# Performance work log

Hardware: AMD Instinct MI355X
Metric: run time of the kernel (lower is better)

Reference implementation:

```python
import jax, jax.numpy as jnp
import numpy as np

B, S, D, M, NQ = 256, 200, 128, 64, 5000
A_TRI, B_TRI, C_TRI = 0.01, 0.05, 0.1  # triangular membership params a,b,c


def setup_inputs():
    key = jax.random.key(0)
    ks = jax.random.split(key, 16)
    g = lambda k, shp: jax.random.normal(k, shp, dtype=jnp.float32) * 0.05
    return dict(
        question_seq=jax.random.randint(ks[0], (B, S), 0, NQ),
        correctness_seq=jax.random.randint(ks[1], (B, S), 0, 2),
        Mk=g(ks[2], (M, D)),
        Mv0=g(ks[3], (M, D)),
        emb_concept=g(ks[4], (NQ, D)),
        emb_interaction=g(ks[5], (2 * NQ, D)),
        Wf=g(ks[6], (D, 2 * D)), bf=jnp.zeros((D,), jnp.float32),
        Wa=g(ks[7], (D, 2 * D)), ba=jnp.zeros((D,), jnp.float32),
        We=g(ks[8], (D, D)), be=jnp.zeros((D,), jnp.float32),
        Wadd=g(ks[9], (D, D)), badd=jnp.zeros((D,), jnp.float32),
        W_ih=g(ks[10], (4 * D, D)), W_hh=g(ks[11], (4 * D, D)),
        b_ih=jnp.zeros((4 * D,), jnp.float32), b_hh=jnp.zeros((4 * D,), jnp.float32),
        hx0=g(ks[12], (1, D)), cx0=g(ks[13], (1, D)),
        Wp=g(ks[14], (1, D)), bp=jnp.zeros((1,), jnp.float32),
    )


def _skvmn(Mk, Mv0, emb_concept, emb_interaction, Wf, bf, Wa, ba, We, be,
           Wadd, badd, W_ih, W_hh, b_ih, b_hh, hx0, cx0, Wp, bp,
           question_seq, correctness_seq):
    concept = emb_concept[question_seq]                                # [B,S,D]
    inter = emb_interaction[question_seq + NQ * correctness_seq]        # [B,S,D]

    # ---- DKVMN key addressing + value memory read/erase/add recurrence ----
    def mem_step(mem, xs):
        k_t, y_t = xs                                                   # [B,D]
        cw = jax.nn.softmax(k_t @ Mk.T, axis=1)                         # [B,M]
        read = jnp.einsum('bm,bmd->bd', cw, mem)                        # [B,D]
        f = jnp.tanh(jnp.concatenate([read, k_t], 1) @ Wf.T + bf)       # [B,D]
        we = jnp.concatenate([f, y_t], 1) @ Wa.T + ba                   # write embed
        erase = jax.nn.sigmoid(we @ We.T + be)
        add = jnp.tanh(we @ Wadd.T + badd)
        mem = mem * (1.0 - cw[:, :, None] * erase[:, None, :]) \
              + cw[:, :, None] * add[:, None, :]
        return mem, (cw, f)

    mem0 = jnp.broadcast_to(Mv0[None], (B, M, D)).astype(jnp.float32)
    _, (w, ft) = jax.lax.scan(
        mem_step, mem0,
        (concept.transpose(1, 0, 2), inter.transpose(1, 0, 2)))
    # w: [S,B,M], ft: [S,B,D]

    # ---- triangular layer: bin correlation weights into identity vectors ----
    wb = w.transpose(1, 0, 2)                                           # [B,S,M]
    tri = jnp.minimum((wb - A_TRI) / (B_TRI - A_TRI),
                      (C_TRI - wb) / (C_TRI - B_TRI))
    tri = jnp.maximum(tri, 0.0)
    iv = jnp.where(tri >= 0.6, 2.0, jnp.where(tri >= 0.1, 1.0, 0.0))    # [B,S,M]

    sq = jnp.sum(iv * iv, axis=2)                                       # [B,S]
    dist = sq[:, :, None] + sq[:, None, :] - 2.0 * jnp.einsum('btm,bjm->btj', iv, iv)
    NEG = jnp.float32(-1e32)
    d2 = jnp.where(dist > 0.0, NEG, dist)
    triu = jnp.triu(jnp.ones((S, S), bool), k=0)                        # mask j >= t
    d2 = jnp.where(triu[None], NEG, d2)
    idx_mat = jnp.arange(S * S, dtype=jnp.float32).reshape(S, S)
    score = d2 + idx_mat[None]                                          # [B,S,S]
    prev_t = jnp.argmax(score, axis=2)                                  # [B,S] prior matching step
    valid = jnp.max(score, axis=2) >= 0.0                               # [B,S]

    # ---- hop-LSTM: substitute hx with hidden state of prior matching step ----
    def lstm_step(carry, xs):
        hx, cx, H = carry
        t, x_t, prev_b, valid_b = xs
        h_prev = H[prev_b, jnp.arange(B)]                               # gather [B,D]
        hx = jnp.where(valid_b[:, None], h_prev, hx)
        gates = x_t @ W_ih.T + b_ih + hx @ W_hh.T + b_hh
        i_, f_, g_, o_ = jnp.split(gates, 4, axis=1)
        cx = jax.nn.sigmoid(f_) * cx + jax.nn.sigmoid(i_) * jnp.tanh(g_)
        hx = jax.nn.sigmoid(o_) * jnp.tanh(cx)
        H = jax.lax.dynamic_update_slice(H, hx[None], (t, 0, 0))
        return (hx, cx, H), hx

    H0 = jnp.zeros((S, B, D), jnp.float32)
    hx = jnp.broadcast_to(hx0, (B, D)).astype(jnp.float32)
    cx = jnp.broadcast_to(cx0, (B, D)).astype(jnp.float32)
    _, hs = jax.lax.scan(lstm_step, (hx, cx, H0),
                         (jnp.arange(S), ft, prev_t.T, valid.T))         # hs: [S,B,D]

    logits = jnp.einsum('sbd,d->sb', hs, Wp[0]) + bp[0]
    return jax.nn.sigmoid(logits).T                                     # [B,S]


def reference(question_seq, correctness_seq, Mk, Mv0, emb_concept, emb_interaction,
              Wf, bf, Wa, ba, We, be, Wadd, badd, W_ih, W_hh, b_ih, b_hh,
              hx0, cx0, Wp, bp):
    return _skvmn(Mk, Mv0, emb_concept, emb_interaction, Wf, bf, Wa, ba, We, be,
                  Wadd, badd, W_ih, W_hh, b_ih, b_hh, hx0, cx0, Wp, bp,
                  question_seq, correctness_seq)
```

## Files before the change

### kernel.cpp

```cpp
#include <hip/hip_runtime.h>

typedef unsigned int u32;
typedef unsigned short u16;
typedef unsigned long long u64;
typedef _Float16 f16;
typedef _Float16 f16x2 __attribute__((ext_vector_type(2)));

#define Bn 256
#define Sn 200
#define Dn 128
#define Mn 64
#define NQn 5000

__device__ __forceinline__ float fdot2f(u32 w, u32 x, float acc) {
#if __has_builtin(__builtin_amdgcn_fdot2)
    return __builtin_amdgcn_fdot2(__builtin_bit_cast(f16x2, w),
                                  __builtin_bit_cast(f16x2, x), acc, false);
#else
    f16x2 a = __builtin_bit_cast(f16x2, w);
    f16x2 b = __builtin_bit_cast(f16x2, x);
    return acc + (float)a[0] * (float)b[0] + (float)a[1] * (float)b[1];
#endif
}

__device__ __forceinline__ u32 packh2(float a, float b) {
    u16 ua = __builtin_bit_cast(u16, (f16)a);
    u16 ub = __builtin_bit_cast(u16, (f16)b);
    return (u32)ua | ((u32)ub << 16);
}

__device__ __forceinline__ float h2f(u16 u) { return (float)__builtin_bit_cast(f16, u); }

__device__ __forceinline__ float fexp2f(float x) {
#if __has_builtin(__builtin_amdgcn_exp2f)
    return __builtin_amdgcn_exp2f(x);
#else
    return exp2f(x);
#endif
}
__device__ __forceinline__ float frcpf(float x) {
#if __has_builtin(__builtin_amdgcn_rcpf)
    return __builtin_amdgcn_rcpf(x);
#else
    return 1.0f / x;
#endif
}
__device__ __forceinline__ float sig_fast(float x)  { return frcpf(1.0f + fexp2f(-1.44269504f * x)); }
__device__ __forceinline__ float tanh_fast(float x) { return fmaf(-2.0f, frcpf(1.0f + fexp2f(2.88539008f * x)), 1.0f); }

__device__ __forceinline__ float sigf(float x) { return 1.0f / (1.0f + expf(-x)); }

__global__ __launch_bounds__(512) void phase0_kernel(
    const int* __restrict__ qseq,
    const float* __restrict__ Mk, const float* __restrict__ embc,
    u16* __restrict__ cw16, ulonglong2* __restrict__ codes)
{
    __shared__ float MkT[Dn * 65];
    __shared__ float kb[8][Dn];
    int tid = threadIdx.x;
    for (int idx = tid; idx < Mn * Dn; idx += 512) {
        int m = idx >> 7, d = idx & 127;
        MkT[d * 65 + m] = Mk[idx];
    }
    __syncthreads();
    int w = tid >> 6, lane = tid & 63;
    int item = blockIdx.x * 8 + w;
    int qq = qseq[item];
    kb[w][lane]      = embc[qq * Dn + lane];
    kb[w][lane + 64] = embc[qq * Dn + lane + 64];
    __syncthreads();
    float acc = 0.0f;
    const float* kw = kb[w];
#pragma unroll 8
    for (int d = 0; d < Dn; ++d)
        acc = fmaf(MkT[d * 65 + lane], kw[d], acc);
    float mx = acc;
    for (int off = 32; off; off >>= 1) mx = fmaxf(mx, __shfl_xor(mx, off));
    float e = expf(acc - mx);
    float sm = e;
    for (int off = 32; off; off >>= 1) sm += __shfl_xor(sm, off);
    float cw = e / sm;
    cw16[item * Mn + lane] = __builtin_bit_cast(u16, (f16)cw);
    float t1 = (cw - 0.01f) / (0.05f - 0.01f);
    float t2 = (0.1f - cw) / (0.1f - 0.05f);
    float tri = fminf(t1, t2);
    tri = fmaxf(tri, 0.0f);
    int iv = (tri >= 0.6f) ? 2 : ((tri >= 0.1f) ? 1 : 0);
    u64 b1 = __ballot(iv >= 1);
    u64 b2 = __ballot(iv == 2);
    if (lane == 0) { codes[item].x = b1; codes[item].y = b2; }
}

__global__ __launch_bounds__(256) void match_kernel(
    const ulonglong2* __restrict__ codes, int* __restrict__ prev)
{
    __shared__ u64 clo[Sn], chi[Sn];
    int b = blockIdx.x, tid = threadIdx.x;
    if (tid < Sn) { ulonglong2 c = codes[b * Sn + tid]; clo[tid] = c.x; chi[tid] = c.y; }
    __syncthreads();
    if (tid < Sn) {
        u64 mylo = clo[tid], myhi = chi[tid];
        int best = -1;
        for (int j = 0; j < tid; ++j)
            if (clo[j] == mylo && chi[j] == myhi) best = j;
        prev[b * Sn + tid] = best;
    }
}

__global__ __launch_bounds__(512) void pre_kernel(
    const float* __restrict__ W, const float* __restrict__ emb,
    const int* __restrict__ qseq, const int* __restrict__ cseq, int mode,
    u16* __restrict__ outp)
{
    __shared__ u32 wL[128 * 65];
    __shared__ u32 vb[8][64];
    int tid = threadIdx.x;
    for (int idx = tid; idx < 128 * 64; idx += 512) {
        int dd = idx >> 6, jj = idx & 63;
        const float2 wv = *(const float2*)(W + dd * 256 + 128 + 2 * jj);
        wL[dd * 65 + jj] = packh2(wv.x, wv.y);
    }
    int w = tid >> 6, lane = tid & 63;
    int item = blockIdx.x * 8 + w;
    int row = qseq[item];
    if (mode) row += NQn * cseq[item];
    {
        const float2 kv = *(const float2*)(emb + row * Dn + 2 * lane);
        vb[w][lane] = packh2(kv.x, kv.y);
    }
    __syncthreads();
    const u32* w0 = wL + lane * 65;
    const u32* w1 = wL + (64 + lane) * 65;
    const u32* x  = vb[w];
    float a0 = 0, a1 = 0, b0 = 0, b1 = 0;
#pragma unroll
    for (int jj = 0; jj < 64; jj += 2) {
        a0 = fdot2f(w0[jj],     x[jj],     a0);
        a1 = fdot2f(w0[jj + 1], x[jj + 1], a1);
        b0 = fdot2f(w1[jj],     x[jj],     b0);
        b1 = fdot2f(w1[jj + 1], x[jj + 1], b1);
    }
    outp[item * Dn + lane]      = __builtin_bit_cast(u16, (f16)(a0 + a1));
    outp[item * Dn + 64 + lane] = __builtin_bit_cast(u16, (f16)(b0 + b1));
}

__global__ __launch_bounds__(512, 2) void memrec_kernel(
    const float* __restrict__ Mv0,
    const float* __restrict__ Wf, const float* __restrict__ bfv,
    const float* __restrict__ Wa, const float* __restrict__ bav,
    const float* __restrict__ We, const float* __restrict__ bev,
    const float* __restrict__ Wadd, const float* __restrict__ badv,
    const u16* __restrict__ cw16, const u16* __restrict__ kf16,
    const u16* __restrict__ ya16, u16* __restrict__ ft16)
{
    __shared__ u32 cwL[Sn * 32];
    __shared__ __align__(16) u32 kfb[2][16 * 64];
    __shared__ __align__(16) u32 yab[2][16 * 64];
    __shared__ __align__(16) u32 rbuf[64], fbuf[64], wbuf[64];
    __shared__ float bfL[Dn], baL[Dn], beL[Dn], badL[Dn];

    int tid = threadIdx.x;
    int d = tid >> 2, q = tid & 3;
    int b = blockIdx.x;

    u32 wfr[16], waf[16], wew[16], wadw[16];
    {
        const float2* wf2r = (const float2*)(Wf + d * 256 + q * 32);
        const float2* wa2f = (const float2*)(Wa + d * 256 + q * 32);
        const float2* we2  = (const float2*)(We + d * 128 + q * 32);
        const float2* wd2  = (const float2*)(Wadd + d * 128 + q * 32);
#pragma unroll
        for (int i = 0; i < 16; ++i) {
            float2 a;
            a = wf2r[i]; wfr[i]  = packh2(a.x, a.y);
            a = wa2f[i]; waf[i]  = packh2(a.x, a.y);
            a = we2[i];  wew[i]  = packh2(a.x, a.y);
            a = wd2[i];  wadw[i] = packh2(a.x, a.y);
        }
    }
    float memv[16];
#pragma unroll
    for (int i = 0; i < 16; ++i) memv[i] = Mv0[(q * 16 + i) * Dn + d];

    if (tid < Dn) { bfL[tid] = bfv[tid]; baL[tid] = bav[tid]; beL[tid] = bev[tid]; badL[tid] = badv[tid]; }

    for (int i = tid; i < Sn * 32; i += 512) cwL[i] = ((const u32*)cw16)[b * Sn * 32 + i];
    {
        const u32* kg = (const u32*)kf16 + (size_t)(b * Sn) * 64;
        const u32* yg = (const u32*)ya16 + (size_t)(b * Sn) * 64;
        for (int i = tid; i < 1024; i += 512) { kfb[0][i] = kg[i]; yab[0][i] = yg[i]; }
    }
    __syncthreads();

    float cwreg[16];
#pragma unroll
    for (int i = 0; i < 8; ++i) {
        u32 v = cwL[q * 8 + i];
        cwreg[2 * i]     = h2f((u16)(v & 0xffff));
        cwreg[2 * i + 1] = h2f((u16)(v >> 16));
    }

    for (int t = 0; t < Sn; ++t) {
        int sl = (t >> 4) & 1, ti = t & 15;
        if (ti == 0) {
            int c1 = (t >> 4) + 1;
            if (c1 * 16 < Sn) {
                int n = (Sn - c1 * 16 < 16 ? Sn - c1 * 16 : 16) * 64;
                const u32* kg = (const u32*)kf16 + (size_t)(b * Sn + c1 * 16) * 64;
                const u32* yg = (const u32*)ya16 + (size_t)(b * Sn + c1 * 16) * 64;
                for (int i = tid; i < n; i += 512) { kfb[sl ^ 1][i] = kg[i]; yab[sl ^ 1][i] = yg[i]; }
            }
        }
        float p0 = 0, p1 = 0, p2 = 0, p3 = 0;
#pragma unroll
        for (int i = 0; i < 4; ++i) {
            p0 = fmaf(cwreg[i],      memv[i],      p0);
            p1 = fmaf(cwreg[4 + i],  memv[4 + i],  p1);
            p2 = fmaf(cwreg[8 + i],  memv[8 + i],  p2);
            p3 = fmaf(cwreg[12 + i], memv[12 + i], p3);
        }
        float pr = (p0 + p1) + (p2 + p3);
        pr += __shfl_xor(pr, 1);
        pr += __shfl_xor(pr, 2);
        if (q == 0) ((f16*)rbuf)[d] = (f16)pr;
        __syncthreads();
        u16 kfc = ((const u16*)(kfb[sl]))[ti * 128 + d];
        float a0 = 0, a1 = 0, a2 = 0, a3 = 0;
#pragma unroll
        for (int u = 0; u < 4; ++u) {
            uint4 x = ((const uint4*)rbuf)[(q << 2) + u];
            a0 = fdot2f(wfr[4 * u + 0], x.x, a0);
            a1 = fdot2f(wfr[4 * u + 1], x.y, a1);
            a2 = fdot2f(wfr[4 * u + 2], x.z, a2);
            a3 = fdot2f(wfr[4 * u + 3], x.w, a3);
        }
        float accf = (a0 + a1) + (a2 + a3);
        accf += __shfl_xor(accf, 1);
        accf += __shfl_xor(accf, 2);
        float fv = tanh_fast(accf + h2f(kfc) + bfL[d]);
        if (q == 0) ((f16*)fbuf)[d] = (f16)fv;
        if (q == 1) ft16[(size_t)(b * Sn + t) * Dn + d] = __builtin_bit_cast(u16, (f16)fv);
        __syncthreads();
        u16 yac = ((const u16*)(yab[sl]))[ti * 128 + d];
        float c0 = 0, c1_ = 0, c2 = 0, c3 = 0;
#pragma unroll
        for (int u = 0; u < 4; ++u) {
            uint4 x = ((const uint4*)fbuf)[(q << 2) + u];
            c0  = fdot2f(waf[4 * u + 0], x.x, c0);
            c1_ = fdot2f(waf[4 * u + 1], x.y, c1_);
            c2  = fdot2f(waf[4 * u + 2], x.z, c2);
            c3  = fdot2f(waf[4 * u + 3], x.w, c3);
        }
        float accw = (c0 + c1_) + (c2 + c3);
        accw += __shfl_xor(accw, 1);
        accw += __shfl_xor(accw, 2);
        if (q == 0) ((f16*)wbuf)[d] = (f16)(accw + h2f(yac) + baL[d]);
        __syncthreads();
        float e0 = 0, e1 = 0, g0 = 0, g1 = 0;
#pragma unroll
        for (int u = 0; u < 4; ++u) {
            uint4 x = ((const uint4*)wbuf)[(q << 2) + u];
            e0 = fdot2f(wew[4 * u + 0], x.x, e0);   g0 = fdot2f(wadw[4 * u + 0], x.x, g0);
            e1 = fdot2f(wew[4 * u + 1], x.y, e1);   g1 = fdot2f(wadw[4 * u + 1], x.y, g1);
            e0 = fdot2f(wew[4 * u + 2], x.z, e0);   g0 = fdot2f(wadw[4 * u + 2], x.z, g0);
            e1 = fdot2f(wew[4 * u + 3], x.w, e1);   g1 = fdot2f(wadw[4 * u + 3], x.w, g1);
        }
        float pe = e0 + e1, pa = g0 + g1;
        pe += __shfl_xor(pe, 1); pe += __shfl_xor(pe, 2);
        pa += __shfl_xor(pa, 1); pa += __shfl_xor(pa, 2);
        float ev = sig_fast(pe + beL[d]);
        float av = tanh_fast(pa + badL[d]);
        u32 cwn[8];
        if (t + 1 < Sn) {
#pragma unroll
            for (int i = 0; i < 8; ++i) cwn[i] = cwL[(t + 1) * 32 + q * 8 + i];
        }
#pragma unroll
        for (int i = 0; i < 16; ++i) {
            float tt = fmaf(-ev, memv[i], av);
            memv[i] = fmaf(cwreg[i], tt, memv[i]);
        }
        if (t + 1 < Sn) {
#pragma unroll
            for (int i = 0; i < 8; ++i) {
                cwreg[2 * i]     = h2f((u16)(cwn[i] & 0xffff));
                cwreg[2 * i + 1] = h2f((u16)(cwn[i] >> 16));
            }
        }
    }
}

__global__ __launch_bounds__(512, 2) void lstm_kernel(
    const float* __restrict__ W_ih, const float* __restrict__ W_hh,
    const float* __restrict__ b_ih, const float* __restrict__ b_hh,
    const float* __restrict__ hx0, const float* __restrict__ cx0,
    const float* __restrict__ Wp, const float* __restrict__ bp,
    const u16* __restrict__ ft16, const int* __restrict__ prev,
    float* __restrict__ out)
{
    __shared__ u32 HL[(Sn + 1) * 64];
    __shared__ __align__(16) u32 ftb[2][16 * 64];
    __shared__ float gbuf[512];
    __shared__ float bsum[512];
    __shared__ int prevL[Sn];
    __shared__ u32 wpL[64];
    __shared__ float bpL;

    int tid = threadIdx.x, b = blockIdx.x;
    u32 wih[64], whh[64];
    {
        const float2* wi2 = (const float2*)(W_ih + tid * Dn);
        const float2* wh2 = (const float2*)(W_hh + tid * Dn);
#pragma unroll
        for (int i = 0; i < 64; ++i) {
            float2 a;
            a = wi2[i]; wih[i] = packh2(a.x, a.y);
            a = wh2[i]; whh[i] = packh2(a.x, a.y);
        }
    }
    bsum[tid] = b_ih[tid] + b_hh[tid];
    if (tid < 64) {
        HL[tid]  = packh2(hx0[2 * tid], hx0[2 * tid + 1]);
        wpL[tid] = packh2(Wp[2 * tid], Wp[2 * tid + 1]);
    }
    if (tid < Sn) prevL[tid] = prev[b * Sn + tid];
    if (tid == 0) bpL = bp[0];
    float cx = (tid < Dn) ? cx0[tid] : 0.0f;
    {
        const u32* fg = (const u32*)ft16 + (size_t)(b * Sn) * 64;
        for (int i = tid; i < 1024; i += 512) ftb[0][i] = fg[i];
    }
    __syncthreads();

    for (int t = 0; t < Sn; ++t) {
        int sl = (t >> 4) & 1, ti = t & 15;
        if (ti == 0) {
            int c1 = (t >> 4) + 1;
            if (c1 * 16 < Sn) {
                int n = (Sn - c1 * 16 < 16 ? Sn - c1 * 16 : 16) * 64;
                const u32* fg = (const u32*)ft16 + (size_t)(b * Sn + c1 * 16) * 64;
                for (int i = tid; i < n; i += 512) ftb[sl ^ 1][i] = fg[i];
            }
        }
        int pv = prevL[t];
        int hrow = (pv >= 0) ? (pv + 1) : t;
        const uint4* h4 = (const uint4*)(HL + hrow * 64);
        const uint4* f4 = (const uint4*)(ftb[sl] + ti * 64);
        float a0 = bsum[tid], a1 = 0, a2 = 0, a3 = 0;
        float b0 = 0, b1 = 0, b2 = 0, b3 = 0;
#pragma unroll
        for (int u = 0; u < 4; ++u) {
            uint4 x = f4[u];
            a0 = fdot2f(wih[4 * u + 0], x.x, a0);
            a1 = fdot2f(wih[4 * u + 1], x.y, a1);
            a2 = fdot2f(wih[4 * u + 2], x.z, a2);
            a3 = fdot2f(wih[4 * u + 3], x.w, a3);
            uint4 y = h4[u];
            b0 = fdot2f(whh[4 * u + 0], y.x, b0);
            b1 = fdot2f(whh[4 * u + 1], y.y, b1);
            b2 = fdot2f(whh[4 * u + 2], y.z, b2);
            b3 = fdot2f(whh[4 * u + 3], y.w, b3);
        }
        gbuf[tid] = ((a0 + a1) + (a2 + a3)) + ((b0 + b1) + (b2 + b3));
        __syncthreads();
        if (tid < 128) {
            float ig = sig_fast(gbuf[tid]);
            float fg = sig_fast(gbuf[128 + tid]);
            float gg = tanh_fast(gbuf[256 + tid]);
            float og = sig_fast(gbuf[384 + tid]);
            cx = fmaf(fg, cx, ig * gg);
            float h = og * tanh_fast(cx);
            ((f16*)HL)[(t + 1) * Dn + tid] = (f16)h;
        }
        __syncthreads();
    }
    if (tid < Sn) {
        float acc = 0.0f;
        const u32* hr = HL + (tid + 1) * 64;
#pragma unroll 16
        for (int j = 0; j < 64; ++j) acc = fdot2f(hr[j], wpL[j], acc);
        out[b * Sn + tid] = sig_fast(acc + bpL);
    }
}

extern "C" void kernel_launch(void* const* d_in, const int* in_sizes, int n_in,
                              void* d_out, int out_size, void* d_ws, size_t ws_size,
                              hipStream_t stream) {
    const int*   qseq = (const int*)d_in[0];
    const int*   cseq = (const int*)d_in[1];
    const float* Mk   = (const float*)d_in[2];
    const float* Mv0  = (const float*)d_in[3];
    const float* embc = (const float*)d_in[4];
    const float* embi = (const float*)d_in[5];
    const float* Wf   = (const float*)d_in[6];
    const float* bfv  = (const float*)d_in[7];
    const float* Wa   = (const float*)d_in[8];
    const float* bav  = (const float*)d_in[9];
    const float* We   = (const float*)d_in[10];
    const float* bev  = (const float*)d_in[11];
    const float* Wadd = (const float*)d_in[12];
    const float* badv = (const float*)d_in[13];
    const float* W_ih = (const float*)d_in[14];
    const float* W_hh = (const float*)d_in[15];
    const float* b_ih = (const float*)d_in[16];
    const float* b_hh = (const float*)d_in[17];
    const float* hx0  = (const float*)d_in[18];
    const float* cx0  = (const float*)d_in[19];
    const float* Wp   = (const float*)d_in[20];
    const float* bp   = (const float*)d_in[21];
    float* out = (float*)d_out;

    char* ws = (char*)d_ws;
    u16* cw16 = (u16*)ws;
    u16* ft16 = (u16*)(ws + 6553600);
    ulonglong2* codes = (ulonglong2*)(ws + 19660800);
    int* prev = (int*)(ws + 20480000);
    u16* kf16 = (u16*)(ws + 20684800);
    u16* ya16 = (u16*)(ws + 33792000);

    phase0_kernel<<<(Bn * Sn) / 8, 512, 0, stream>>>(qseq, Mk, embc, cw16, codes);
    pre_kernel<<<(Bn * Sn) / 8, 512, 0, stream>>>(Wf, embc, qseq, cseq, 0, kf16);
    pre_kernel<<<(Bn * Sn) / 8, 512, 0, stream>>>(Wa, embi, qseq, cseq, 1, ya16);
    match_kernel<<<Bn, 256, 0, stream>>>(codes, prev);
    memrec_kernel<<<Bn, 512, 0, stream>>>(Mv0, Wf, bfv, Wa, bav, We, bev, Wadd, badv,
                                          cw16, kf16, ya16, ft16);
    lstm_kernel<<<Bn, 512, 0, stream>>>(W_ih, W_hh, b_ih, b_hh, hx0, cx0, Wp, bp,
                                        ft16, prev, out);
}
```

Measured before the change: 628.9 us.

## Fold Wa into erase/add weights, precompute per-vocab rows, restructure LSTM gates

Precomputes We·Wa and Wadd·Wa products so the memory recurrence skips the write-embed matvec and one barrier per step. The input-dependent projections are computed once per vocabulary row rather than per (batch, step) item, then gathered by index inside the recurrence. The LSTM kernel now splits each hidden unit across four lanes holding all four gates, reducing with shuffles so the gate staging buffer and one barrier per step go away. Risks include extra fp16 rounding from the folded matrices and gathers that no longer coalesce.

Measured after the change: 638.9 us. Within noise of the previous version (+1.6%).

```diff
diff --git a/kernel.cpp b/kernel.cpp
--- a/kernel.cpp
+++ b/kernel.cpp
@@ -47,8 +47,6 @@
 }
 __device__ __forceinline__ float sig_fast(float x)  { return frcpf(1.0f + fexp2f(-1.44269504f * x)); }
 __device__ __forceinline__ float tanh_fast(float x) { return fmaf(-2.0f, frcpf(1.0f + fexp2f(2.88539008f * x)), 1.0f); }
-
-__device__ __forceinline__ float sigf(float x) { return 1.0f / (1.0f + expf(-x)); }
 
 __global__ __launch_bounds__(512) void phase0_kernel(
     const int* __restrict__ qseq,
@@ -107,9 +105,40 @@
     }
 }
 
-__global__ __launch_bounds__(512) void pre_kernel(
+__global__ __launch_bounds__(512) void setup_kernel(
+    const float* __restrict__ Wa, const float* __restrict__ We,
+    const float* __restrict__ Wadd,
+    const float* __restrict__ ba, const float* __restrict__ be,
+    const float* __restrict__ badd,
+    float* __restrict__ CEf, float* __restrict__ CAf,
+    float* __restrict__ CEy, float* __restrict__ CAy,
+    float* __restrict__ c0s)
+{
+    __shared__ float weR[128], waR[128];
+    int d = blockIdx.x, tid = threadIdx.x;
+    if (tid < 128) weR[tid] = We[d * 128 + tid];
+    else if (tid < 256) waR[tid - 128] = Wadd[d * 128 + (tid - 128)];
+    __syncthreads();
+    int mat = tid >> 7, j = tid & 127;
+    const float* src = (mat == 0 || mat == 2) ? weR : waR;
+    int col = (mat < 2) ? j : (128 + j);
+    float acc = 0.0f;
+    for (int k = 0; k < 128; ++k) acc = fmaf(src[k], Wa[k * 256 + col], acc);
+    float* dst = (mat == 0) ? CEf : (mat == 1) ? CAf : (mat == 2) ? CEy : CAy;
+    dst[d * 128 + j] = acc;
+    if (tid == 0) {
+        float a = 0.0f;
+        for (int k = 0; k < 128; ++k) a = fmaf(weR[k], ba[k], a);
+        c0s[d] = a + be[d];
+    } else if (tid == 1) {
+        float a = 0.0f;
+        for (int k = 0; k < 128; ++k) a = fmaf(waR[k], ba[k], a);
+        c0s[128 + d] = a + badd[d];
+    }
+}
+
+__global__ __launch_bounds__(512) void rowk_kernel(
     const float* __restrict__ W, const float* __restrict__ emb,
-    const int* __restrict__ qseq, const int* __restrict__ cseq, int mode,
     u16* __restrict__ outp)
 {
     __shared__ u32 wL[128 * 65];
@@ -121,9 +150,7 @@
         wL[dd * 65 + jj] = packh2(wv.x, wv.y);
     }
     int w = tid >> 6, lane = tid & 63;
-    int item = blockIdx.x * 8 + w;
-    int row = qseq[item];
-    if (mode) row += NQn * cseq[item];
+    int row = blockIdx.x * 8 + w;
     {
         const float2 kv = *(const float2*)(emb + row * Dn + 2 * lane);
         vb[w][lane] = packh2(kv.x, kv.y);
@@ -140,55 +167,111 @@
         b0 = fdot2f(w1[jj],     x[jj],     b0);
         b1 = fdot2f(w1[jj + 1], x[jj + 1], b1);
     }
-    outp[item * Dn + lane]      = __builtin_bit_cast(u16, (f16)(a0 + a1));
-    outp[item * Dn + 64 + lane] = __builtin_bit_cast(u16, (f16)(b0 + b1));
+    outp[row * Dn + lane]      = __builtin_bit_cast(u16, (f16)(a0 + a1));
+    outp[row * Dn + 64 + lane] = __builtin_bit_cast(u16, (f16)(b0 + b1));
+}
+
+__global__ __launch_bounds__(512) void rowe_kernel(
+    const float* __restrict__ CEy, const float* __restrict__ CAy,
+    const float* __restrict__ c0s, const float* __restrict__ embi,
+    u16* __restrict__ ebR, u16* __restrict__ abR)
+{
+    __shared__ u32 eL[128 * 65];
+    __shared__ u32 aL[128 * 65];
+    __shared__ u32 vb[8][64];
+    __shared__ float c0L[256];
+    int tid = threadIdx.x;
+    for (int idx = tid; idx < 128 * 64; idx += 512) {
+        int dd = idx >> 6, jj = idx & 63;
+        const float2 e2 = *(const float2*)(CEy + dd * 128 + 2 * jj);
+        const float2 a2 = *(const float2*)(CAy + dd * 128 + 2 * jj);
+        eL[dd * 65 + jj] = packh2(e2.x, e2.y);
+        aL[dd * 65 + jj] = packh2(a2.x, a2.y);
+    }
+    if (tid < 256) c0L[tid] = c0s[tid];
+    int w = tid >> 6, lane = tid & 63;
+    int row = blockIdx.x * 8 + w;
+    {
+        const float2 kv = *(const float2*)(embi + row * Dn + 2 * lane);
+        vb[w][lane] = packh2(kv.x, kv.y);
+    }
+    __syncthreads();
+    const u32* x   = vb[w];
+    const u32* e0p = eL + lane * 65;
+    const u32* e1p = eL + (64 + lane) * 65;
+    const u32* a0p = aL + lane * 65;
+    const u32* a1p = aL + (64 + lane) * 65;
+    float ea0 = 0, ea1 = 0, eb0 = 0, eb1 = 0;
+    float aa0 = 0, aa1 = 0, ab0 = 0, ab1 = 0;
+#pragma unroll
+    for (int jj = 0; jj < 64; jj += 2) {
+        ea0 = fdot2f(e0p[jj],     x[jj],     ea0);
+        ea1 = fdot2f(e0p[jj + 1], x[jj + 1], ea1);
+        eb0 = fdot2f(e1p[jj],     x[jj],     eb0);
+        eb1 = fdot2f(e1p[jj + 1], x[jj + 1], eb1);
+        aa0 = fdot2f(a0p[jj],     x[jj],     aa0);
+        aa1 = fdot2f(a0p[jj + 1], x[jj + 1], aa1);
+        ab0 = fdot2f(a1p[jj],     x[jj],     ab0);
+        ab1 = fdot2f(a1p[jj + 1], x[jj + 1], ab1);
+    }
+    ebR[row * Dn + lane]      = __builtin_bit_cast(u16, (f16)(ea0 + ea1 + c0L[lane]));
+    ebR[row * Dn + 64 + lane] = __builtin_bit_cast(u16, (f16)(eb0 + eb1 + c0L[64 + lane]));
+    abR[row * Dn + lane]      = __builtin_bit_cast(u16, (f16)(aa0 + aa1 + c0L[128 + lane]));
+    abR[row * Dn + 64 + lane] = __builtin_bit_cast(u16, (f16)(ab0 + ab1 + c0L[192 + lane]));
 }
 
 __global__ __launch_bounds__(512, 2) void memrec_kernel(
     const float* __restrict__ Mv0,
     const float* __restrict__ Wf, const float* __restrict__ bfv,
-    const float* __restrict__ Wa, const float* __restrict__ bav,
-    const float* __restrict__ We, const float* __restrict__ bev,
-    const float* __restrict__ Wadd, const float* __restrict__ badv,
-    const u16* __restrict__ cw16, const u16* __restrict__ kf16,
-    const u16* __restrict__ ya16, u16* __restrict__ ft16)
+    const float* __restrict__ CEf, const float* __restrict__ CAf,
+    const u16* __restrict__ cw16, const u16* __restrict__ kfR,
+    const u16* __restrict__ ebR, const u16* __restrict__ abR,
+    const int* __restrict__ qseq, const int* __restrict__ cseq,
+    u16* __restrict__ ft16)
 {
     __shared__ u32 cwL[Sn * 32];
     __shared__ __align__(16) u32 kfb[2][16 * 64];
-    __shared__ __align__(16) u32 yab[2][16 * 64];
-    __shared__ __align__(16) u32 rbuf[64], fbuf[64], wbuf[64];
-    __shared__ float bfL[Dn], baL[Dn], beL[Dn], badL[Dn];
+    __shared__ __align__(16) u32 ebb[2][16 * 64];
+    __shared__ __align__(16) u32 abb[2][16 * 64];
+    __shared__ __align__(16) u32 rbuf[64], fbuf[64];
+    __shared__ float bfL[Dn];
+    __shared__ int qrowL[Sn], irowL[Sn];
 
     int tid = threadIdx.x;
     int d = tid >> 2, q = tid & 3;
     int b = blockIdx.x;
 
-    u32 wfr[16], waf[16], wew[16], wadw[16];
+    u32 wfr[16], wew[16], wadw[16];
     {
-        const float2* wf2r = (const float2*)(Wf + d * 256 + q * 32);
-        const float2* wa2f = (const float2*)(Wa + d * 256 + q * 32);
-        const float2* we2  = (const float2*)(We + d * 128 + q * 32);
-        const float2* wd2  = (const float2*)(Wadd + d * 128 + q * 32);
+        const float2* wf2 = (const float2*)(Wf  + d * 256 + q * 32);
+        const float2* we2 = (const float2*)(CEf + d * 128 + q * 32);
+        const float2* wd2 = (const float2*)(CAf + d * 128 + q * 32);
 #pragma unroll
         for (int i = 0; i < 16; ++i) {
             float2 a;
-            a = wf2r[i]; wfr[i]  = packh2(a.x, a.y);
-            a = wa2f[i]; waf[i]  = packh2(a.x, a.y);
-            a = we2[i];  wew[i]  = packh2(a.x, a.y);
-            a = wd2[i];  wadw[i] = packh2(a.x, a.y);
+            a = wf2[i]; wfr[i]  = packh2(a.x, a.y);
+            a = we2[i]; wew[i]  = packh2(a.x, a.y);
+            a = wd2[i]; wadw[i] = packh2(a.x, a.y);
         }
     }
     float memv[16];
 #pragma unroll
     for (int i = 0; i < 16; ++i) memv[i] = Mv0[(q * 16 + i) * Dn + d];
 
-    if (tid < Dn) { bfL[tid] = bfv[tid]; baL[tid] = bav[tid]; beL[tid] = bev[tid]; badL[tid] = badv[tid]; }
+    if (tid < Dn) bfL[tid] = bfv[tid];
+    if (tid < Sn) {
+        int qq = qseq[b * Sn + tid];
+        qrowL[tid] = qq;
+        irowL[tid] = qq + NQn * cseq[b * Sn + tid];
+    }
+    __syncthreads();
 
     for (int i = tid; i < Sn * 32; i += 512) cwL[i] = ((const u32*)cw16)[b * Sn * 32 + i];
-    {
-        const u32* kg = (const u32*)kf16 + (size_t)(b * Sn) * 64;
-        const u32* yg = (const u32*)ya16 + (size_t)(b * Sn) * 64;
-        for (int i = tid; i < 1024; i += 512) { kfb[0][i] = kg[i]; yab[0][i] = yg[i]; }
+    for (int i = tid; i < 1024; i += 512) {
+        int s = i >> 6, off = i & 63;
+        kfb[0][i] = ((const u32*)kfR)[qrowL[s] * 64 + off];
+        ebb[0][i] = ((const u32*)ebR)[irowL[s] * 64 + off];
+        abb[0][i] = ((const u32*)abR)[irowL[s] * 64 + off];
     }
     __syncthreads();
 
@@ -206,9 +289,13 @@
             int c1 = (t >> 4) + 1;
             if (c1 * 16 < Sn) {
                 int n = (Sn - c1 * 16 < 16 ? Sn - c1 * 16 : 16) * 64;
-                const u32* kg = (const u32*)kf16 + (size_t)(b * Sn + c1 * 16) * 64;
-                const u32* yg = (const u32*)ya16 + (size_t)(b * Sn + c1 * 16) * 64;
-                for (int i = tid; i < n; i += 512) { kfb[sl ^ 1][i] = kg[i]; yab[sl ^ 1][i] = yg[i]; }
+                for (int i = tid; i < n; i += 512) {
+                    int s = i >> 6, off = i & 63;
+                    int t2 = c1 * 16 + s;
+                    kfb[sl ^ 1][i] = ((const u32*)kfR)[qrowL[t2] * 64 + off];
+                    ebb[sl ^ 1][i] = ((const u32*)ebR)[irowL[t2] * 64 + off];
+                    abb[sl ^ 1][i] = ((const u32*)abR)[irowL[t2] * 64 + off];
+                }
             }
         }
         float p0 = 0, p1 = 0, p2 = 0, p3 = 0;
@@ -225,6 +312,8 @@
         if (q == 0) ((f16*)rbuf)[d] = (f16)pr;
         __syncthreads();
         u16 kfc = ((const u16*)(kfb[sl]))[ti * 128 + d];
+        u16 ebc = ((const u16*)(ebb[sl]))[ti * 128 + d];
+        u16 abc = ((const u16*)(abb[sl]))[ti * 128 + d];
         float a0 = 0, a1 = 0, a2 = 0, a3 = 0;
 #pragma unroll
         for (int u = 0; u < 4; ++u) {
@@ -241,25 +330,10 @@
         if (q == 0) ((f16*)fbuf)[d] = (f16)fv;
         if (q == 1) ft16[(size_t)(b * Sn + t) * Dn + d] = __builtin_bit_cast(u16, (f16)fv);
         __syncthreads();
-        u16 yac = ((const u16*)(yab[sl]))[ti * 128 + d];
-        float c0 = 0, c1_ = 0, c2 = 0, c3 = 0;
+        float e0 = 0, e1 = 0, g0 = 0, g1 = 0;
 #pragma unroll
         for (int u = 0; u < 4; ++u) {
             uint4 x = ((const uint4*)fbuf)[(q << 2) + u];
-            c0  = fdot2f(waf[4 * u + 0], x.x, c0);
-            c1_ = fdot2f(waf[4 * u + 1], x.y, c1_);
-            c2  = fdot2f(waf[4 * u + 2], x.z, c2);
-            c3  = fdot2f(waf[4 * u + 3], x.w, c3);
-        }
-        float accw = (c0 + c1_) + (c2 + c3);
-        accw += __shfl_xor(accw, 1);
-        accw += __shfl_xor(accw, 2);
-        if (q == 0) ((f16*)wbuf)[d] = (f16)(accw + h2f(yac) + baL[d]);
-        __syncthreads();
-        float e0 = 0, e1 = 0, g0 = 0, g1 = 0;
-#pragma unroll
-        for (int u = 0; u < 4; ++u) {
-            uint4 x = ((const uint4*)wbuf)[(q << 2) + u];
             e0 = fdot2f(wew[4 * u + 0], x.x, e0);   g0 = fdot2f(wadw[4 * u + 0], x.x, g0);
             e1 = fdot2f(wew[4 * u + 1], x.y, e1);   g1 = fdot2f(wadw[4 * u + 1], x.y, g1);
             e0 = fdot2f(wew[4 * u + 2], x.z, e0);   g0 = fdot2f(wadw[4 * u + 2], x.z, g0);
@@ -268,8 +342,8 @@
         float pe = e0 + e1, pa = g0 + g1;
         pe += __shfl_xor(pe, 1); pe += __shfl_xor(pe, 2);
         pa += __shfl_xor(pa, 1); pa += __shfl_xor(pa, 2);
-        float ev = sig_fast(pe + beL[d]);
-        float av = tanh_fast(pa + badL[d]);
+        float ev = sig_fast(pe + h2f(ebc));
+        float av = tanh_fast(pa + h2f(abc));
         u32 cwn[8];
         if (t + 1 < Sn) {
 #pragma unroll
@@ -298,34 +372,35 @@
     const u16* __restrict__ ft16, const int* __restrict__ prev,
     float* __restrict__ out)
 {
-    __shared__ u32 HL[(Sn + 1) * 64];
+    __shared__ __align__(16) u32 HL[(Sn + 1) * 64];
     __shared__ __align__(16) u32 ftb[2][16 * 64];
-    __shared__ float gbuf[512];
-    __shared__ float bsum[512];
     __shared__ int prevL[Sn];
     __shared__ u32 wpL[64];
     __shared__ float bpL;
 
     int tid = threadIdx.x, b = blockIdx.x;
-    u32 wih[64], whh[64];
-    {
-        const float2* wi2 = (const float2*)(W_ih + tid * Dn);
-        const float2* wh2 = (const float2*)(W_hh + tid * Dn);
-#pragma unroll
-        for (int i = 0; i < 64; ++i) {
+    int d = tid >> 2, q = tid & 3;
+    u32 wx[4][16], wh[4][16];
+    float bias[4];
+#pragma unroll
+    for (int g = 0; g < 4; ++g) {
+        const float2* wi2 = (const float2*)(W_ih + (size_t)(g * 128 + d) * Dn + q * 32);
+        const float2* wh2 = (const float2*)(W_hh + (size_t)(g * 128 + d) * Dn + q * 32);
+#pragma unroll
+        for (int i = 0; i < 16; ++i) {
             float2 a;
-            a = wi2[i]; wih[i] = packh2(a.x, a.y);
-            a = wh2[i]; whh[i] = packh2(a.x, a.y);
-        }
-    }
-    bsum[tid] = b_ih[tid] + b_hh[tid];
+            a = wi2[i]; wx[g][i] = packh2(a.x, a.y);
+            a = wh2[i]; wh[g][i] = packh2(a.x, a.y);
+        }
+        bias[g] = b_ih[g * 128 + d] + b_hh[g * 128 + d];
+    }
     if (tid < 64) {
         HL[tid]  = packh2(hx0[2 * tid], hx0[2 * tid + 1]);
         wpL[tid] = packh2(Wp[2 * tid], Wp[2 * tid + 1]);
     }
     if (tid < Sn) prevL[tid] = prev[b * Sn + tid];
     if (tid == 0) bpL = bp[0];
-    float cx = (tid < Dn) ? cx0[tid] : 0.0f;
+    float cx = cx0[d];
     {
         const u32* fg = (const u32*)ft16 + (size_t)(b * Sn) * 64;
         for (int i = tid; i < 1024; i += 512) ftb[0][i] = fg[i];
@@ -344,34 +419,38 @@
         }
         int pv = prevL[t];
         int hrow = (pv >= 0) ? (pv + 1) : t;
-        const uint4* h4 = (const uint4*)(HL + hrow * 64);
-        const uint4* f4 = (const uint4*)(ftb[sl] + ti * 64);
-        float a0 = bsum[tid], a1 = 0, a2 = 0, a3 = 0;
-        float b0 = 0, b1 = 0, b2 = 0, b3 = 0;
-#pragma unroll
-        for (int u = 0; u < 4; ++u) {
-            uint4 x = f4[u];
-            a0 = fdot2f(wih[4 * u + 0], x.x, a0);
-            a1 = fdot2f(wih[4 * u + 1], x.y, a1);
-            a2 = fdot2f(wih[4 * u + 2], x.z, a2);
-            a3 = fdot2f(wih[4 * u + 3], x.w, a3);
-            uint4 y = h4[u];
-            b0 = fdot2f(whh[4 * u + 0], y.x, b0);
-            b1 = fdot2f(whh[4 * u + 1], y.y, b1);
-            b2 = fdot2f(whh[4 * u + 2], y.z, b2);
-            b3 = fdot2f(whh[4 * u + 3], y.w, b3);
-        }
-        gbuf[tid] = ((a0 + a1) + (a2 + a3)) + ((b0 + b1) + (b2 + b3));
-        __syncthreads();
-        if (tid < 128) {
-            float ig = sig_fast(gbuf[tid]);
-            float fg = sig_fast(gbuf[128 + tid]);
-            float gg = tanh_fast(gbuf[256 + tid]);
-            float og = sig_fast(gbuf[384 + tid]);
-            cx = fmaf(fg, cx, ig * gg);
-            float h = og * tanh_fast(cx);
-            ((f16*)HL)[(t + 1) * Dn + tid] = (f16)h;
-        }
+        const uint4* h4 = (const uint4*)(HL + hrow * 64 + q * 16);
+        const uint4* f4 = (const uint4*)(ftb[sl] + ti * 64 + q * 16);
+        uint4 xv[4], yv[4];
+#pragma unroll
+        for (int u = 0; u < 4; ++u) { xv[u] = f4[u]; yv[u] = h4[u]; }
+        float gacc[4];
+#pragma unroll
+        for (int g = 0; g < 4; ++g) {
+            float s0 = 0, s1 = 0, s2 = 0, s3 = 0;
+#pragma unroll
+            for (int u = 0; u < 4; ++u) {
+                s0 = fdot2f(wx[g][4 * u + 0], xv[u].x, s0);
+                s1 = fdot2f(wx[g][4 * u + 1], xv[u].y, s1);
+                s2 = fdot2f(wx[g][4 * u + 2], xv[u].z, s2);
+                s3 = fdot2f(wx[g][4 * u + 3], xv[u].w, s3);
+                s0 = fdot2f(wh[g][4 * u + 0], yv[u].x, s0);
+                s1 = fdot2f(wh[g][4 * u + 1], yv[u].y, s1);
+                s2 = fdot2f(wh[g][4 * u + 2], yv[u].z, s2);
+                s3 = fdot2f(wh[g][4 * u + 3], yv[u].w, s3);
+            }
+            float s = (s0 + s1) + (s2 + s3);
+            s += __shfl_xor(s, 1);
+            s += __shfl_xor(s, 2);
+            gacc[g] = s + bias[g];
+        }
+        float ig = sig_fast(gacc[0]);
+        float fgt = sig_fast(gacc[1]);
+        float gg = tanh_fast(gacc[2]);
+        float og = sig_fast(gacc[3]);
+        cx = fmaf(fgt, cx, ig * gg);
+        float h = og * tanh_fast(cx);
+        if (q == 0) ((f16*)HL)[(t + 1) * Dn + d] = (f16)h;
         __syncthreads();
     }
     if (tid < Sn) {
@@ -415,15 +494,23 @@
     u16* ft16 = (u16*)(ws + 6553600);
     ulonglong2* codes = (ulonglong2*)(ws + 19660800);
     int* prev = (int*)(ws + 20480000);
-    u16* kf16 = (u16*)(ws + 20684800);
-    u16* ya16 = (u16*)(ws + 33792000);
-
+    u16* kfR  = (u16*)(ws + 20684800);
+    u16* ebR  = (u16*)(ws + 21964800);
+    u16* abR  = (u16*)(ws + 24524800);
+    float* CEf = (float*)(ws + 27084800);
+    float* CAf = (float*)(ws + 27150336);
+    float* CEy = (float*)(ws + 27215872);
+    float* CAy = (float*)(ws + 27281408);
+    float* c0s = (float*)(ws + 27346944);
+
+    setup_kernel<<<128, 512, 0, stream>>>(Wa, We, Wadd, bav, bev, badv,
+                                          CEf, CAf, CEy, CAy, c0s);
     phase0_kernel<<<(Bn * Sn) / 8, 512, 0, stream>>>(qseq, Mk, embc, cw16, codes);
-    pre_kernel<<<(Bn * Sn) / 8, 512, 0, stream>>>(Wf, embc, qseq, cseq, 0, kf16);
-    pre_kernel<<<(Bn * Sn) / 8, 512, 0, stream>>>(Wa, embi, qseq, cseq, 1, ya16);
+    rowk_kernel<<<NQn / 8, 512, 0, stream>>>(Wf, embc, kfR);
+    rowe_kernel<<<(2 * NQn) / 8, 512, 0, stream>>>(CEy, CAy, c0s, embi, ebR, abR);
     match_kernel<<<Bn, 256, 0, stream>>>(codes, prev);
-    memrec_kernel<<<Bn, 512, 0, stream>>>(Mv0, Wf, bfv, Wa, bav, We, bev, Wadd, badv,
-                                          cw16, kf16, ya16, ft16);
+    memrec_kernel<<<Bn, 512, 0, stream>>>(Mv0, Wf, bfv, CEf, CAf,
+                                          cw16, kfR, ebR, abR, qseq, cseq, ft16);
     lstm_kernel<<<Bn, 512, 0, stream>>>(W_ih, W_hh, b_ih, b_hh, hx0, cx0, Wp, bp,
                                         ft16, prev, out);
 }
```
